# Performance work log

Measured on AMD Instinct MI355X. Metric: run time of the kernel, lower is better.

The kernel has to match this reference:

```python
import jax, jax.numpy as jnp
import numpy as np

N, F = 8192, 128
NEG_INF = -9e15
LEAKY_ALPHA = 0.2

def setup_inputs() -> dict:
    key = jax.random.key(0)
    k1, k2, k3, k4 = jax.random.split(key, 4)
    x = jax.random.normal(k1, (N, F), dtype=jnp.float32)
    h0 = jax.random.normal(k2, (N, F), dtype=jnp.float32)
    # sparse-ish binary adjacency (density ~0.005) with self-loops so every row has a neighbor
    adj = (jax.random.uniform(k3, (N, N)) < 0.005).astype(jnp.float32)
    diag = jnp.arange(N)
    adj = adj.at[diag, diag].set(1.0)
    # xavier_uniform-ish init for attention vector a [2F, 1]
    limit = float(np.sqrt(6.0 / (2 * F + 1)) * 1.414)
    a = jax.random.uniform(k4, (2 * F, 1), minval=-limit, maxval=limit, dtype=jnp.float32)
    temp = jnp.zeros((5,), dtype=jnp.float32)  # reset_parameters fills 0 -> coe = 0.5
    return {"x": x, "h0": h0, "adj": adj, "a": a, "temp": temp, "lamda": 1, "l": 1}


def reference(x, h0, adj, a, temp, lamda, l):
    # beta = log(lamda/l + 1) is computed in the original but never used in the output math.
    f = x.shape[1]
    # GAT-style scores: e[i,j] = leakyrelu(x_i.a1 + x_j.a2)
    feat_1 = x @ a[:f]          # [N, 1]
    feat_2 = x @ a[f:]          # [N, 1]
    e = jax.nn.leaky_relu(feat_1 + feat_2.T, negative_slope=LEAKY_ALPHA)  # [N, N]
    att = jnp.where(adj > 0, e, NEG_INF)
    U = jax.nn.softmax(att, axis=1)          # [N, N]
    prop_u = U @ x                           # [N, F]
    rowsum = jnp.sum(0.5 * U * U, axis=1)    # [N]  (sum of U*P, P = 0.5*U)
    coe = jax.nn.sigmoid(temp)
    # forward lifting
    xi = x * rowsum[:, None]
    feat_odd = prop_u - xi
    feat_even = x + prop_u - xi
    feat = coe[2] * feat_odd + (1.0 - coe[2]) * feat_even
    # inverse lifting
    prop_u2 = U @ feat
    odd = feat - prop_u2
    even = coe[3] * prop_u2 + odd * rowsum[:, None]
    feat_prime = coe[1] * even + (1.0 - coe[1]) * odd
    return 0.2 * feat_prime + 0.8 * h0
```

## Files before the change

### kernel.cpp

```cpp
#include <hip/hip_runtime.h>
#include <math.h>

#define NN 8192
#define FF 128
#define CAP 128

typedef float nfloat4 __attribute__((ext_vector_type(4)));

__global__ __launch_bounds__(256) void k_scores(const float* __restrict__ x,
                                                const float* __restrict__ a,
                                                float* __restrict__ f1,
                                                float* __restrict__ f2) {
  int gid = blockIdx.x * blockDim.x + threadIdx.x;
  int row = gid >> 6;
  int lane = gid & 63;
  if (row >= NN) return;
  const float* xr = x + (size_t)row * FF;
  float v0 = xr[lane], v1 = xr[lane + 64];
  float s1 = v0 * a[lane] + v1 * a[lane + 64];
  float s2 = v0 * a[FF + lane] + v1 * a[FF + lane + 64];
  #pragma unroll
  for (int off = 32; off > 0; off >>= 1) {
    s1 += __shfl_down(s1, off);
    s2 += __shfl_down(s2, off);
  }
  if (lane == 0) { f1[row] = s1; f2[row] = s2; }
}

__global__ __launch_bounds__(256) void k_scan(const float* __restrict__ adj,
                                              int* __restrict__ nnzg,
                                              int* __restrict__ colsg) {
  const int row = blockIdx.x;
  const int t = threadIdx.x;
  const int lane = t & 63, w = t >> 6;
  __shared__ int s_cnt[32];

  const nfloat4* arow = (const nfloat4*)(adj + (size_t)row * NN);
  unsigned msk[8];
  int within[8];
  const unsigned long long lt = (1ull << lane) - 1ull;
  #pragma unroll
  for (int it = 0; it < 8; ++it) {
    nfloat4 v = __builtin_nontemporal_load(&arow[it * 256 + t]);
    bool c0 = v.x > 0.f, c1 = v.y > 0.f, c2 = v.z > 0.f, c3 = v.w > 0.f;
    unsigned long long b0 = __ballot(c0), b1 = __ballot(c1),
                       b2 = __ballot(c2), b3 = __ballot(c3);
    within[it] = __popcll(b0 & lt) + __popcll(b1 & lt) +
                 __popcll(b2 & lt) + __popcll(b3 & lt);
    msk[it] = (c0 ? 1u : 0u) | (c1 ? 2u : 0u) | (c2 ? 4u : 0u) | (c3 ? 8u : 0u);
    if (lane == 0)
      s_cnt[it * 4 + w] = __popcll(b0) + __popcll(b1) + __popcll(b2) + __popcll(b3);
  }
  __syncthreads();

  int base[8];
  int run = 0;
  #pragma unroll
  for (int it = 0; it < 8; ++it) {
    #pragma unroll
    for (int ww = 0; ww < 4; ++ww) {
      if (ww == w) base[it] = run;
      run += s_cnt[it * 4 + ww];
    }
  }
  if (t == 0) nnzg[row] = run < CAP ? run : CAP;

  int* cg = colsg + (size_t)row * CAP;
  #pragma unroll
  for (int it = 0; it < 8; ++it) {
    unsigned m = msk[it];
    if (m) {
      int pos = base[it] + within[it];
      int j0 = (it * 256 + t) * 4;
      if (m & 1u) { if (pos < CAP) cg[pos] = j0;     pos++; }
      if (m & 2u) { if (pos < CAP) cg[pos] = j0 + 1; pos++; }
      if (m & 4u) { if (pos < CAP) cg[pos] = j0 + 2; pos++; }
      if (m & 8u) { if (pos < CAP) cg[pos] = j0 + 3; pos++; }
    }
  }
}

__global__ __launch_bounds__(256) void k_fwd(
    const float* __restrict__ x,
    const float* __restrict__ f1g, const float* __restrict__ f2g,
    const float* __restrict__ temp,
    const int* __restrict__ nnzg, const int* __restrict__ colsg,
    float* __restrict__ valsg, float* __restrict__ rowsumg,
    float* __restrict__ featg) {
  const int wl = threadIdx.x >> 6;
  const int lane = threadIdx.x & 63;
  const int row = blockIdx.x * 4 + wl;

  __shared__ int   s_c[4][CAP];
  __shared__ float s_u[4][CAP];

  const int cnt = nnzg[row];
  const int* cg = colsg + (size_t)row * CAP;
  const int i0 = lane, i1 = lane + 64;
  int col0 = (i0 < cnt) ? cg[i0] : 0;
  int col1 = (i1 < cnt) ? cg[i1] : 0;

  const float F1 = f1g[row];
  float e0 = -INFINITY, e1 = -INFINITY;
  if (i0 < cnt) { float s = F1 + f2g[col0]; e0 = s > 0.f ? s : 0.2f * s; }
  if (i1 < cnt) { float s = F1 + f2g[col1]; e1 = s > 0.f ? s : 0.2f * s; }
  float mx = fmaxf(e0, e1);
  #pragma unroll
  for (int off = 32; off > 0; off >>= 1) mx = fmaxf(mx, __shfl_xor(mx, off));
  float p0 = (i0 < cnt) ? expf(e0 - mx) : 0.f;
  float p1 = (i1 < cnt) ? expf(e1 - mx) : 0.f;
  float sm = p0 + p1;
  #pragma unroll
  for (int off = 32; off > 0; off >>= 1) sm += __shfl_xor(sm, off);
  float inv = 1.f / sm;
  float u0 = p0 * inv, u1 = p1 * inv;
  float q = u0 * u0 + u1 * u1;
  #pragma unroll
  for (int off = 32; off > 0; off >>= 1) q += __shfl_xor(q, off);
  float rs = 0.5f * q;

  if (i0 < cnt) { s_c[wl][i0] = col0; s_u[wl][i0] = u0; }
  if (i1 < cnt) { s_c[wl][i1] = col1; s_u[wl][i1] = u1; }
  float* vg = valsg + (size_t)row * CAP;
  if (i0 < cnt) vg[i0] = u0;
  if (i1 < cnt) vg[i1] = u1;
  if (lane == 0) rowsumg[row] = rs;
  __syncthreads();

  float acc0 = 0.f, acc1 = 0.f;
  int k = 0;
  for (; k + 3 < cnt; k += 4) {
    int   c0 = s_c[wl][k],   c1 = s_c[wl][k+1], c2 = s_c[wl][k+2], c3 = s_c[wl][k+3];
    float w0 = s_u[wl][k],   w1 = s_u[wl][k+1], w2 = s_u[wl][k+2], w3 = s_u[wl][k+3];
    float a0 = x[(size_t)c0 * FF + lane],      b0 = x[(size_t)c0 * FF + lane + 64];
    float a1 = x[(size_t)c1 * FF + lane],      b1 = x[(size_t)c1 * FF + lane + 64];
    float a2 = x[(size_t)c2 * FF + lane],      b2 = x[(size_t)c2 * FF + lane + 64];
    float a3 = x[(size_t)c3 * FF + lane],      b3 = x[(size_t)c3 * FF + lane + 64];
    acc0 += w0 * a0 + w1 * a1 + w2 * a2 + w3 * a3;
    acc1 += w0 * b0 + w1 * b1 + w2 * b2 + w3 * b3;
  }
  for (; k < cnt; ++k) {
    int c = s_c[wl][k]; float u = s_u[wl][k];
    acc0 += u * x[(size_t)c * FF + lane];
    acc1 += u * x[(size_t)c * FF + lane + 64];
  }

  const float coe2 = 1.f / (1.f + expf(-temp[2]));
  float xv0 = x[(size_t)row * FF + lane];
  float xv1 = x[(size_t)row * FF + lane + 64];
  featg[(size_t)row * FF + lane]      = acc0 - xv0 * rs + (1.f - coe2) * xv0;
  featg[(size_t)row * FF + lane + 64] = acc1 - xv1 * rs + (1.f - coe2) * xv1;
}

__global__ __launch_bounds__(256) void k_bwd(
    const float* __restrict__ featg, const float* __restrict__ h0,
    const float* __restrict__ temp,
    const int* __restrict__ nnzg, const int* __restrict__ colsg,
    const float* __restrict__ valsg, const float* __restrict__ rowsumg,
    float* __restrict__ out) {
  const int wl = threadIdx.x >> 6;
  const int lane = threadIdx.x & 63;
  const int row = blockIdx.x * 4 + wl;

  __shared__ int   s_c[4][CAP];
  __shared__ float s_u[4][CAP];

  const int cnt = nnzg[row];
  const int* cg = colsg + (size_t)row * CAP;
  const float* vg = valsg + (size_t)row * CAP;
  const int i0 = lane, i1 = lane + 64;
  if (i0 < cnt) { s_c[wl][i0] = cg[i0]; s_u[wl][i0] = vg[i0]; }
  if (i1 < cnt) { s_c[wl][i1] = cg[i1]; s_u[wl][i1] = vg[i1]; }
  __syncthreads();

  float acc0 = 0.f, acc1 = 0.f;
  int k = 0;
  for (; k + 3 < cnt; k += 4) {
    int   c0 = s_c[wl][k],   c1 = s_c[wl][k+1], c2 = s_c[wl][k+2], c3 = s_c[wl][k+3];
    float w0 = s_u[wl][k],   w1 = s_u[wl][k+1], w2 = s_u[wl][k+2], w3 = s_u[wl][k+3];
    float a0 = featg[(size_t)c0 * FF + lane],  b0 = featg[(size_t)c0 * FF + lane + 64];
    float a1 = featg[(size_t)c1 * FF + lane],  b1 = featg[(size_t)c1 * FF + lane + 64];
    float a2 = featg[(size_t)c2 * FF + lane],  b2 = featg[(size_t)c2 * FF + lane + 64];
    float a3 = featg[(size_t)c3 * FF + lane],  b3 = featg[(size_t)c3 * FF + lane + 64];
    acc0 += w0 * a0 + w1 * a1 + w2 * a2 + w3 * a3;
    acc1 += w0 * b0 + w1 * b1 + w2 * b2 + w3 * b3;
  }
  for (; k < cnt; ++k) {
    int c = s_c[wl][k]; float u = s_u[wl][k];
    acc0 += u * featg[(size_t)c * FF + lane];
    acc1 += u * featg[(size_t)c * FF + lane + 64];
  }

  const float rs = rowsumg[row];
  const float coe1 = 1.f / (1.f + expf(-temp[1]));
  const float coe3 = 1.f / (1.f + expf(-temp[3]));
  float ft0 = featg[(size_t)row * FF + lane];
  float ft1 = featg[(size_t)row * FF + lane + 64];
  float odd0 = ft0 - acc0, odd1 = ft1 - acc1;
  float ev0 = coe3 * acc0 + odd0 * rs;
  float ev1 = coe3 * acc1 + odd1 * rs;
  float fp0 = coe1 * ev0 + (1.f - coe1) * odd0;
  float fp1 = coe1 * ev1 + (1.f - coe1) * odd1;
  out[(size_t)row * FF + lane]      = 0.2f * fp0 + 0.8f * h0[(size_t)row * FF + lane];
  out[(size_t)row * FF + lane + 64] = 0.2f * fp1 + 0.8f * h0[(size_t)row * FF + lane + 64];
}

extern "C" void kernel_launch(void* const* d_in, const int* in_sizes, int n_in,
                              void* d_out, int out_size, void* d_ws, size_t ws_size,
                              hipStream_t stream) {
  const float* x    = (const float*)d_in[0];
  const float* h0   = (const float*)d_in[1];
  const float* adj  = (const float*)d_in[2];
  const float* a    = (const float*)d_in[3];
  const float* temp = (const float*)d_in[4];
  float* out = (float*)d_out;

  float* f1 = (float*)d_ws;
  float* f2 = f1 + NN;
  float* rowsum = f2 + NN;
  int*   nnz = (int*)(rowsum + NN);
  int*   cols = nnz + NN;
  float* vals = (float*)(cols + (size_t)NN * CAP);
  float* feat = vals + (size_t)NN * CAP;

  k_scores<<<NN / 4, 256, 0, stream>>>(x, a, f1, f2);
  k_scan<<<NN, 256, 0, stream>>>(adj, nnz, cols);
  k_fwd<<<NN / 4, 256, 0, stream>>>(x, f1, f2, temp, nnz, cols, vals, rowsum, feat);
  k_bwd<<<NN / 4, 256, 0, stream>>>(feat, h0, temp, nnz, cols, vals, rowsum, out);
}
```

Baseline: 84.53 us.

## Fuse adjacency scan into forward SpMM kernel with per-wave row compaction

Merges the adjacency scan and forward aggregation kernels: each wavefront now scans one full adjacency row with a running ballot-based prefix and writes the compacted column list straight into shared memory. This removes the global round trip of the column indices and one kernel launch. Separately, the gather loops in both SpMM kernels are unrolled from 4 to 8 neighbors for more memory-level parallelism, and the h0/out accesses use nontemporal loads and stores. The trade-off is that each row's 32 KB scan becomes serial within one wave instead of being spread over a 256-thread block, which may reduce memory parallelism on the dominant adjacency read.

```diff
diff --git a/kernel.cpp b/kernel.cpp
--- a/kernel.cpp
+++ b/kernel.cpp
@@ -27,80 +27,44 @@
   if (lane == 0) { f1[row] = s1; f2[row] = s2; }
 }
 
-__global__ __launch_bounds__(256) void k_scan(const float* __restrict__ adj,
-                                              int* __restrict__ nnzg,
-                                              int* __restrict__ colsg) {
-  const int row = blockIdx.x;
-  const int t = threadIdx.x;
-  const int lane = t & 63, w = t >> 6;
-  __shared__ int s_cnt[32];
+__global__ __launch_bounds__(256) void k_scanfwd(
+    const float* __restrict__ adj, const float* __restrict__ x,
+    const float* __restrict__ f1g, const float* __restrict__ f2g,
+    const float* __restrict__ temp,
+    int* __restrict__ nnzg, int* __restrict__ colsg, float* __restrict__ valsg,
+    float* __restrict__ rowsumg, float* __restrict__ featg) {
+  const int w = threadIdx.x >> 6;
+  const int lane = threadIdx.x & 63;
+  const int row = blockIdx.x * 4 + w;
+
+  __shared__ int   s_c[4][CAP];
+  __shared__ float s_u[4][CAP];
 
   const nfloat4* arow = (const nfloat4*)(adj + (size_t)row * NN);
-  unsigned msk[8];
-  int within[8];
   const unsigned long long lt = (1ull << lane) - 1ull;
-  #pragma unroll
-  for (int it = 0; it < 8; ++it) {
-    nfloat4 v = __builtin_nontemporal_load(&arow[it * 256 + t]);
+  int run = 0;
+  #pragma unroll 8
+  for (int it = 0; it < 32; ++it) {
+    nfloat4 v = __builtin_nontemporal_load(&arow[it * 64 + lane]);
     bool c0 = v.x > 0.f, c1 = v.y > 0.f, c2 = v.z > 0.f, c3 = v.w > 0.f;
     unsigned long long b0 = __ballot(c0), b1 = __ballot(c1),
                        b2 = __ballot(c2), b3 = __ballot(c3);
-    within[it] = __popcll(b0 & lt) + __popcll(b1 & lt) +
-                 __popcll(b2 & lt) + __popcll(b3 & lt);
-    msk[it] = (c0 ? 1u : 0u) | (c1 ? 2u : 0u) | (c2 ? 4u : 0u) | (c3 ? 8u : 0u);
-    if (lane == 0)
-      s_cnt[it * 4 + w] = __popcll(b0) + __popcll(b1) + __popcll(b2) + __popcll(b3);
-  }
+    int pos = run + __popcll(b0 & lt) + __popcll(b1 & lt) +
+                    __popcll(b2 & lt) + __popcll(b3 & lt);
+    int j0 = (it * 64 + lane) * 4;
+    if (c0) { if (pos < CAP) s_c[w][pos] = j0;     pos++; }
+    if (c1) { if (pos < CAP) s_c[w][pos] = j0 + 1; pos++; }
+    if (c2) { if (pos < CAP) s_c[w][pos] = j0 + 2; pos++; }
+    if (c3) { if (pos < CAP) s_c[w][pos] = j0 + 3; pos++; }
+    run += __popcll(b0) + __popcll(b1) + __popcll(b2) + __popcll(b3);
+  }
+  const int cnt = run < CAP ? run : CAP;
   __syncthreads();
 
-  int base[8];
-  int run = 0;
-  #pragma unroll
-  for (int it = 0; it < 8; ++it) {
-    #pragma unroll
-    for (int ww = 0; ww < 4; ++ww) {
-      if (ww == w) base[it] = run;
-      run += s_cnt[it * 4 + ww];
-    }
-  }
-  if (t == 0) nnzg[row] = run < CAP ? run : CAP;
-
-  int* cg = colsg + (size_t)row * CAP;
-  #pragma unroll
-  for (int it = 0; it < 8; ++it) {
-    unsigned m = msk[it];
-    if (m) {
-      int pos = base[it] + within[it];
-      int j0 = (it * 256 + t) * 4;
-      if (m & 1u) { if (pos < CAP) cg[pos] = j0;     pos++; }
-      if (m & 2u) { if (pos < CAP) cg[pos] = j0 + 1; pos++; }
-      if (m & 4u) { if (pos < CAP) cg[pos] = j0 + 2; pos++; }
-      if (m & 8u) { if (pos < CAP) cg[pos] = j0 + 3; pos++; }
-    }
-  }
-}
-
-__global__ __launch_bounds__(256) void k_fwd(
-    const float* __restrict__ x,
-    const float* __restrict__ f1g, const float* __restrict__ f2g,
-    const float* __restrict__ temp,
-    const int* __restrict__ nnzg, const int* __restrict__ colsg,
-    float* __restrict__ valsg, float* __restrict__ rowsumg,
-    float* __restrict__ featg) {
-  const int wl = threadIdx.x >> 6;
-  const int lane = threadIdx.x & 63;
-  const int row = blockIdx.x * 4 + wl;
-
-  __shared__ int   s_c[4][CAP];
-  __shared__ float s_u[4][CAP];
-
-  const int cnt = nnzg[row];
-  const int* cg = colsg + (size_t)row * CAP;
+  const float F1 = f1g[row];
   const int i0 = lane, i1 = lane + 64;
-  int col0 = (i0 < cnt) ? cg[i0] : 0;
-  int col1 = (i1 < cnt) ? cg[i1] : 0;
-
-  const float F1 = f1g[row];
+  int col0 = (i0 < cnt) ? s_c[w][i0] : 0;
+  int col1 = (i1 < cnt) ? s_c[w][i1] : 0;
   float e0 = -INFINITY, e1 = -INFINITY;
   if (i0 < cnt) { float s = F1 + f2g[col0]; e0 = s > 0.f ? s : 0.2f * s; }
   if (i1 < cnt) { float s = F1 + f2g[col1]; e1 = s > 0.f ? s : 0.2f * s; }
@@ -117,30 +81,34 @@
   float q = u0 * u0 + u1 * u1;
   #pragma unroll
   for (int off = 32; off > 0; off >>= 1) q += __shfl_xor(q, off);
-  float rs = 0.5f * q;
-
-  if (i0 < cnt) { s_c[wl][i0] = col0; s_u[wl][i0] = u0; }
-  if (i1 < cnt) { s_c[wl][i1] = col1; s_u[wl][i1] = u1; }
-  float* vg = valsg + (size_t)row * CAP;
-  if (i0 < cnt) vg[i0] = u0;
-  if (i1 < cnt) vg[i1] = u1;
-  if (lane == 0) rowsumg[row] = rs;
-  __syncthreads();
+  const float rs = 0.5f * q;
+
+  if (i0 < cnt) { s_u[w][i0] = u0; colsg[(size_t)row * CAP + i0] = col0;
+                  valsg[(size_t)row * CAP + i0] = u0; }
+  if (i1 < cnt) { s_u[w][i1] = u1; colsg[(size_t)row * CAP + i1] = col1;
+                  valsg[(size_t)row * CAP + i1] = u1; }
+  if (lane == 0) { nnzg[row] = cnt; rowsumg[row] = rs; }
 
   float acc0 = 0.f, acc1 = 0.f;
   int k = 0;
-  for (; k + 3 < cnt; k += 4) {
-    int   c0 = s_c[wl][k],   c1 = s_c[wl][k+1], c2 = s_c[wl][k+2], c3 = s_c[wl][k+3];
-    float w0 = s_u[wl][k],   w1 = s_u[wl][k+1], w2 = s_u[wl][k+2], w3 = s_u[wl][k+3];
+  for (; k + 7 < cnt; k += 8) {
+    int   c0 = s_c[w][k],   c1 = s_c[w][k+1], c2 = s_c[w][k+2], c3 = s_c[w][k+3];
+    int   c4 = s_c[w][k+4], c5 = s_c[w][k+5], c6 = s_c[w][k+6], c7 = s_c[w][k+7];
+    float w0 = s_u[w][k],   w1 = s_u[w][k+1], w2 = s_u[w][k+2], w3 = s_u[w][k+3];
+    float w4 = s_u[w][k+4], w5 = s_u[w][k+5], w6 = s_u[w][k+6], w7 = s_u[w][k+7];
     float a0 = x[(size_t)c0 * FF + lane],      b0 = x[(size_t)c0 * FF + lane + 64];
     float a1 = x[(size_t)c1 * FF + lane],      b1 = x[(size_t)c1 * FF + lane + 64];
     float a2 = x[(size_t)c2 * FF + lane],      b2 = x[(size_t)c2 * FF + lane + 64];
     float a3 = x[(size_t)c3 * FF + lane],      b3 = x[(size_t)c3 * FF + lane + 64];
-    acc0 += w0 * a0 + w1 * a1 + w2 * a2 + w3 * a3;
-    acc1 += w0 * b0 + w1 * b1 + w2 * b2 + w3 * b3;
+    float a4 = x[(size_t)c4 * FF + lane],      b4 = x[(size_t)c4 * FF + lane + 64];
+    float a5 = x[(size_t)c5 * FF + lane],      b5 = x[(size_t)c5 * FF + lane + 64];
+    float a6 = x[(size_t)c6 * FF + lane],      b6 = x[(size_t)c6 * FF + lane + 64];
+    float a7 = x[(size_t)c7 * FF + lane],      b7 = x[(size_t)c7 * FF + lane + 64];
+    acc0 += w0*a0 + w1*a1 + w2*a2 + w3*a3 + w4*a4 + w5*a5 + w6*a6 + w7*a7;
+    acc1 += w0*b0 + w1*b1 + w2*b2 + w3*b3 + w4*b4 + w5*b5 + w6*b6 + w7*b7;
   }
   for (; k < cnt; ++k) {
-    int c = s_c[wl][k]; float u = s_u[wl][k];
+    int c = s_c[w][k]; float u = s_u[w][k];
     acc0 += u * x[(size_t)c * FF + lane];
     acc1 += u * x[(size_t)c * FF + lane + 64];
   }
@@ -175,15 +143,21 @@
 
   float acc0 = 0.f, acc1 = 0.f;
   int k = 0;
-  for (; k + 3 < cnt; k += 4) {
+  for (; k + 7 < cnt; k += 8) {
     int   c0 = s_c[wl][k],   c1 = s_c[wl][k+1], c2 = s_c[wl][k+2], c3 = s_c[wl][k+3];
+    int   c4 = s_c[wl][k+4], c5 = s_c[wl][k+5], c6 = s_c[wl][k+6], c7 = s_c[wl][k+7];
     float w0 = s_u[wl][k],   w1 = s_u[wl][k+1], w2 = s_u[wl][k+2], w3 = s_u[wl][k+3];
+    float w4 = s_u[wl][k+4], w5 = s_u[wl][k+5], w6 = s_u[wl][k+6], w7 = s_u[wl][k+7];
     float a0 = featg[(size_t)c0 * FF + lane],  b0 = featg[(size_t)c0 * FF + lane + 64];
     float a1 = featg[(size_t)c1 * FF + lane],  b1 = featg[(size_t)c1 * FF + lane + 64];
     float a2 = featg[(size_t)c2 * FF + lane],  b2 = featg[(size_t)c2 * FF + lane + 64];
     float a3 = featg[(size_t)c3 * FF + lane],  b3 = featg[(size_t)c3 * FF + lane + 64];
-    acc0 += w0 * a0 + w1 * a1 + w2 * a2 + w3 * a3;
-    acc1 += w0 * b0 + w1 * b1 + w2 * b2 + w3 * b3;
+    float a4 = featg[(size_t)c4 * FF + lane],  b4 = featg[(size_t)c4 * FF + lane + 64];
+    float a5 = featg[(size_t)c5 * FF + lane],  b5 = featg[(size_t)c5 * FF + lane + 64];
+    float a6 = featg[(size_t)c6 * FF + lane],  b6 = featg[(size_t)c6 * FF + lane + 64];
+    float a7 = featg[(size_t)c7 * FF + lane],  b7 = featg[(size_t)c7 * FF + lane + 64];
+    acc0 += w0*a0 + w1*a1 + w2*a2 + w3*a3 + w4*a4 + w5*a5 + w6*a6 + w7*a7;
+    acc1 += w0*b0 + w1*b1 + w2*b2 + w3*b3 + w4*b4 + w5*b5 + w6*b6 + w7*b7;
   }
   for (; k < cnt; ++k) {
     int c = s_c[wl][k]; float u = s_u[wl][k];
@@ -201,8 +175,10 @@
   float ev1 = coe3 * acc1 + odd1 * rs;
   float fp0 = coe1 * ev0 + (1.f - coe1) * odd0;
   float fp1 = coe1 * ev1 + (1.f - coe1) * odd1;
-  out[(size_t)row * FF + lane]      = 0.2f * fp0 + 0.8f * h0[(size_t)row * FF + lane];
-  out[(size_t)row * FF + lane + 64] = 0.2f * fp1 + 0.8f * h0[(size_t)row * FF + lane + 64];
+  float h00 = __builtin_nontemporal_load(h0 + (size_t)row * FF + lane);
+  float h01 = __builtin_nontemporal_load(h0 + (size_t)row * FF + lane + 64);
+  __builtin_nontemporal_store(0.2f * fp0 + 0.8f * h00, out + (size_t)row * FF + lane);
+  __builtin_nontemporal_store(0.2f * fp1 + 0.8f * h01, out + (size_t)row * FF + lane + 64);
 }
 
 extern "C" void kernel_launch(void* const* d_in, const int* in_sizes, int n_in,
@@ -224,7 +200,6 @@
   float* feat = vals + (size_t)NN * CAP;
 
   k_scores<<<NN / 4, 256, 0, stream>>>(x, a, f1, f2);
-  k_scan<<<NN, 256, 0, stream>>>(adj, nnz, cols);
-  k_fwd<<<NN / 4, 256, 0, stream>>>(x, f1, f2, temp, nnz, cols, vals, rowsum, feat);
+  k_scanfwd<<<NN / 4, 256, 0, stream>>>(adj, x, f1, f2, temp, nnz, cols, vals, rowsum, feat);
   k_bwd<<<NN / 4, 256, 0, stream>>>(feat, h0, temp, nnz, cols, vals, rowsum, out);
 }
```

After: 81.75 us. -3.3%, faster.
